# Optimization experiments

Hardware: AMD Instinct MI355X
Metric: run time of the kernel (lower is better)

The kernel has to match this reference:

```python
import jax, jax.numpy as jnp
import numpy as np

EPS = 1e-5


def setup_inputs() -> dict:
    key = jax.random.key(0)
    k1, k2, k3 = jax.random.split(key, 3)
    B, C, H, W = 64, 512, 28, 28
    G = 8
    x = jax.random.normal(k1, (B, C, H, W), dtype=jnp.float32)
    weight = jax.random.normal(k2, (G,), dtype=jnp.float32)
    bias = jax.random.normal(k3, (G,), dtype=jnp.float32)
    return {"x": x, "weight": weight, "bias": bias, "groups": G}


def reference(x, weight, bias, groups):
    B, C, H, W = x.shape
    G = groups
    cpg = C // G
    hw = H * W
    xg = x.reshape(B, G, cpg, hw)                       # [B,G,cpg,HW]
    # per-channel spatial mean
    means = jnp.mean(xg, axis=-1, keepdims=True)        # [B,G,cpg,1]
    # similarity map: dot product of each spatial vector with channel-mean vector
    s = jnp.sum(xg * means, axis=2)                     # [B,G,HW]
    # normalize s over spatial dim (population variance, eps=1e-5)
    mu = jnp.mean(s, axis=-1, keepdims=True)
    var = jnp.mean(jnp.square(s - mu), axis=-1, keepdims=True)
    t = (s - mu) * jax.lax.rsqrt(var + EPS)             # [B,G,HW]
    gate = jax.nn.sigmoid(t * weight[None, :, None] + bias[None, :, None])
    out = xg * gate[:, :, None, :]                      # broadcast gate over channels
    return out.reshape(B, C, H, W)
```

## Files before the change

kernel.cpp:

```cpp
#include <hip/hip_runtime.h>


#define HW    784
#define HW4   196
#define CPG   64
#define NG    8

__global__ __launch_bounds__(512, 4)
void sge_kernel(const float* __restrict__ x,
                const float* __restrict__ weight,
                const float* __restrict__ bias,
                float* __restrict__ out) {
    __shared__ float means[CPG];
    __shared__ float gate[HW];
    __shared__ float red[16];

    const int t    = threadIdx.x;
    const int lane = t & 63;
    const int wave = t >> 6;
    const int c    = t >> 3;
    const int jj   = t & 7;

    const int bg = blockIdx.x;
    const int g  = bg & (NG - 1);
    const size_t tile4 = (size_t)bg * (CPG * HW4);
    const float4* xp = (const float4*)x + tile4 + (size_t)c * HW4;

    float cs = 0.f;
#pragma unroll
    for (int k = 0; k < 24; ++k) {
        const float4 v = xp[jj + 8 * k];
        cs += (v.x + v.y) + (v.z + v.w);
    }
    if (jj < 4) {
        const float4 v = xp[192 + jj];
        cs += (v.x + v.y) + (v.z + v.w);
    }
    cs += __shfl_xor(cs, 1, 64);
    cs += __shfl_xor(cs, 2, 64);
    cs += __shfl_xor(cs, 4, 64);
    if (jj == 0) means[c] = cs * (1.0f / (float)HW);
    __syncthreads();

    const float* xs = x + (size_t)bg * (CPG * HW);
    const bool  has1 = (t + 512) < HW;
    const int   p1   = has1 ? (t + 512) : t;
    float s0 = 0.f, s1 = 0.f;
#pragma unroll 8
    for (int cc = 0; cc < CPG; ++cc) {
        const float  mc   = means[cc];
        const float* rowp = xs + (size_t)cc * HW;
        s0 += rowp[t]  * mc;
        s1 += rowp[p1] * mc;
    }

    float rs  = s0 + (has1 ? s1 : 0.f);
    float rs2 = s0 * s0 + (has1 ? s1 * s1 : 0.f);
#pragma unroll
    for (int m = 1; m < 64; m <<= 1) {
        rs  += __shfl_xor(rs,  m, 64);
        rs2 += __shfl_xor(rs2, m, 64);
    }
    if (lane == 0) { red[wave] = rs; red[8 + wave] = rs2; }
    __syncthreads();

    float sum_s = 0.f, sum_s2 = 0.f;
#pragma unroll
    for (int w = 0; w < 8; ++w) { sum_s += red[w]; sum_s2 += red[8 + w]; }
    const float mu   = sum_s * (1.0f / (float)HW);
    const float var  = sum_s2 * (1.0f / (float)HW) - mu * mu;
    const float rstd = rsqrtf(var + 1e-5f);
    const float wg   = weight[g];
    const float bgv  = bias[g];

    {
        const float z0 = (s0 - mu) * rstd * wg + bgv;
        gate[t] = 1.0f / (1.0f + __expf(-z0));
        if (has1) {
            const float z1 = (s1 - mu) * rstd * wg + bgv;
            gate[t + 512] = 1.0f / (1.0f + __expf(-z1));
        }
    }
    __syncthreads();

    const float4* g4 = (const float4*)gate;
    float4* op = (float4*)out + tile4 + (size_t)c * HW4;
#pragma unroll
    for (int k = 0; k < 24; ++k) {
        const float4 v  = xp[jj + 8 * k];
        const float4 gv = g4[jj + 8 * k];
        float4 o;
        o.x = v.x * gv.x; o.y = v.y * gv.y;
        o.z = v.z * gv.z; o.w = v.w * gv.w;
        op[jj + 8 * k] = o;
    }
    if (jj < 4) {
        const float4 v  = xp[192 + jj];
        const float4 gv = g4[192 + jj];
        float4 o;
        o.x = v.x * gv.x; o.y = v.y * gv.y;
        o.z = v.z * gv.z; o.w = v.w * gv.w;
        op[192 + jj] = o;
    }
}

extern "C" void kernel_launch(void* const* d_in, const int* in_sizes, int n_in,
                              void* d_out, int out_size, void* d_ws, size_t ws_size,
                              hipStream_t stream) {
    const float* x      = (const float*)d_in[0];
    const float* weight = (const float*)d_in[1];
    const float* bias   = (const float*)d_in[2];
    float* out = (float*)d_out;
    sge_kernel<<<dim3(512), dim3(512), 0, stream>>>(x, weight, bias, out);
}
```

Baseline: 207.0 us.

## Split fused SGE kernel into means, gate, and grid-stride multiply kernels

Replaces the single per-(batch,group) fused kernel, which ran only 512 blocks, with three kernels. One wave computes each channel mean, a per-group kernel computes and stores the gate map in workspace, and a grid-stride elementwise kernel applies the gate using nontemporal stores. The aim is more parallelism and occupancy in the mean and multiply phases. In exchange it adds two kernel launches, a workspace round trip for means and gates, and extra full reads of x that may no longer hit cache.

Result: slower. 227.8 us (+10.0%).

```diff
diff --git a/kernel.cpp b/kernel.cpp
--- a/kernel.cpp
+++ b/kernel.cpp
@@ -5,102 +5,113 @@
 #define HW4   196
 #define CPG   64
 #define NG    8
+#define NROWS (64 * 512)
+#define TOT4  (NROWS * HW4)
 
-__global__ __launch_bounds__(512, 4)
-void sge_kernel(const float* __restrict__ x,
-                const float* __restrict__ weight,
-                const float* __restrict__ bias,
-                float* __restrict__ out) {
-    __shared__ float means[CPG];
-    __shared__ float gate[HW];
-    __shared__ float red[16];
+typedef float f32x4 __attribute__((ext_vector_type(4)));
+
+__global__ __launch_bounds__(256)
+void k_means(const float* __restrict__ x, float* __restrict__ means) {
+    const int t    = threadIdx.x;
+    const int lane = t & 63;
+    const int row  = blockIdx.x * 4 + (t >> 6);
+    const float4* xp = (const float4*)x + (size_t)row * HW4;
+
+    const float4 v0 = xp[lane];
+    const float4 v1 = xp[lane + 64];
+    const float4 v2 = xp[lane + 128];
+    float s = ((v0.x + v0.y) + (v0.z + v0.w))
+            + ((v1.x + v1.y) + (v1.z + v1.w))
+            + ((v2.x + v2.y) + (v2.z + v2.w));
+    if (lane < 4) {
+        const float4 v3 = xp[192 + lane];
+        s += (v3.x + v3.y) + (v3.z + v3.w);
+    }
+#pragma unroll
+    for (int m = 1; m < 64; m <<= 1) s += __shfl_xor(s, m, 64);
+    if (lane == 0) means[row] = s * (1.0f / (float)HW);
+}
+
+__global__ __launch_bounds__(256)
+void k_gate(const float* __restrict__ x, const float* __restrict__ means,
+            const float* __restrict__ weight, const float* __restrict__ bias,
+            float* __restrict__ gate) {
+    __shared__ float mloc[CPG];
+    __shared__ float red[8];
 
     const int t    = threadIdx.x;
     const int lane = t & 63;
     const int wave = t >> 6;
-    const int c    = t >> 3;
-    const int jj   = t & 7;
+    const int bg   = blockIdx.x;
+    const int g    = bg & (NG - 1);
 
-    const int bg = blockIdx.x;
-    const int g  = bg & (NG - 1);
-    const size_t tile4 = (size_t)bg * (CPG * HW4);
-    const float4* xp = (const float4*)x + tile4 + (size_t)c * HW4;
-
-    float cs = 0.f;
-#pragma unroll
-    for (int k = 0; k < 24; ++k) {
-        const float4 v = xp[jj + 8 * k];
-        cs += (v.x + v.y) + (v.z + v.w);
-    }
-    if (jj < 4) {
-        const float4 v = xp[192 + jj];
-        cs += (v.x + v.y) + (v.z + v.w);
-    }
-    cs += __shfl_xor(cs, 1, 64);
-    cs += __shfl_xor(cs, 2, 64);
-    cs += __shfl_xor(cs, 4, 64);
-    if (jj == 0) means[c] = cs * (1.0f / (float)HW);
+    if (t < CPG) mloc[t] = means[bg * CPG + t];
     __syncthreads();
 
     const float* xs = x + (size_t)bg * (CPG * HW);
-    const bool  has1 = (t + 512) < HW;
-    const int   p1   = has1 ? (t + 512) : t;
-    float s0 = 0.f, s1 = 0.f;
+    float s0 = 0.f, s1 = 0.f, s2 = 0.f, s3 = 0.f;
 #pragma unroll 8
-    for (int cc = 0; cc < CPG; ++cc) {
-        const float  mc   = means[cc];
-        const float* rowp = xs + (size_t)cc * HW;
-        s0 += rowp[t]  * mc;
-        s1 += rowp[p1] * mc;
+    for (int c = 0; c < CPG; ++c) {
+        const float  mc = mloc[c];
+        const float* rp = xs + c * HW;
+        s0 += rp[t]       * mc;
+        s1 += rp[t + 256] * mc;
+        s2 += rp[t + 512] * mc;
+        if (t < 16) s3 += rp[t + 768] * mc;
     }
 
-    float rs  = s0 + (has1 ? s1 : 0.f);
-    float rs2 = s0 * s0 + (has1 ? s1 * s1 : 0.f);
+    float rs  = s0 + s1 + s2 + s3;
+    float rs2 = s0 * s0 + s1 * s1 + s2 * s2 + s3 * s3;
 #pragma unroll
     for (int m = 1; m < 64; m <<= 1) {
         rs  += __shfl_xor(rs,  m, 64);
         rs2 += __shfl_xor(rs2, m, 64);
     }
-    if (lane == 0) { red[wave] = rs; red[8 + wave] = rs2; }
+    if (lane == 0) { red[wave] = rs; red[4 + wave] = rs2; }
     __syncthreads();
 
-    float sum_s = 0.f, sum_s2 = 0.f;
-#pragma unroll
-    for (int w = 0; w < 8; ++w) { sum_s += red[w]; sum_s2 += red[8 + w]; }
+    const float sum_s  = red[0] + red[1] + red[2] + red[3];
+    const float sum_s2 = red[4] + red[5] + red[6] + red[7];
     const float mu   = sum_s * (1.0f / (float)HW);
     const float var  = sum_s2 * (1.0f / (float)HW) - mu * mu;
     const float rstd = rsqrtf(var + 1e-5f);
     const float wg   = weight[g];
     const float bgv  = bias[g];
 
+    float* gr = gate + (size_t)bg * HW;
     {
         const float z0 = (s0 - mu) * rstd * wg + bgv;
-        gate[t] = 1.0f / (1.0f + __expf(-z0));
-        if (has1) {
-            const float z1 = (s1 - mu) * rstd * wg + bgv;
-            gate[t + 512] = 1.0f / (1.0f + __expf(-z1));
+        const float z1 = (s1 - mu) * rstd * wg + bgv;
+        const float z2 = (s2 - mu) * rstd * wg + bgv;
+        gr[t]       = 1.0f / (1.0f + __expf(-z0));
+        gr[t + 256] = 1.0f / (1.0f + __expf(-z1));
+        gr[t + 512] = 1.0f / (1.0f + __expf(-z2));
+        if (t < 16) {
+            const float z3 = (s3 - mu) * rstd * wg + bgv;
+            gr[t + 768] = 1.0f / (1.0f + __expf(-z3));
         }
     }
-    __syncthreads();
+}
 
+__global__ __launch_bounds__(256)
+void k_mul(const float* __restrict__ x, const float* __restrict__ gate,
+           float* __restrict__ out) {
+    const int tid    = blockIdx.x * 256 + threadIdx.x;
+    const int stride = gridDim.x * 256;
+    const float4* x4 = (const float4*)x;
     const float4* g4 = (const float4*)gate;
-    float4* op = (float4*)out + tile4 + (size_t)c * HW4;
-#pragma unroll
-    for (int k = 0; k < 24; ++k) {
-        const float4 v  = xp[jj + 8 * k];
-        const float4 gv = g4[jj + 8 * k];
-        float4 o;
+    f32x4*        o4 = (f32x4*)out;
+
+    for (int i = tid; i < TOT4; i += stride) {
+        const int row = i / HW4;
+        const int h4  = i - row * HW4;
+        const int bg  = row >> 6;
+        const float4 v  = x4[i];
+        const float4 gv = g4[bg * HW4 + h4];
+        f32x4 o;
         o.x = v.x * gv.x; o.y = v.y * gv.y;
         o.z = v.z * gv.z; o.w = v.w * gv.w;
-        op[jj + 8 * k] = o;
-    }
-    if (jj < 4) {
-        const float4 v  = xp[192 + jj];
-        const float4 gv = g4[192 + jj];
-        float4 o;
-        o.x = v.x * gv.x; o.y = v.y * gv.y;
-        o.z = v.z * gv.z; o.w = v.w * gv.w;
-        op[192 + jj] = o;
+        __builtin_nontemporal_store(o, &o4[i]);
     }
 }
 
@@ -110,6 +121,11 @@
     const float* x      = (const float*)d_in[0];
     const float* weight = (const float*)d_in[1];
     const float* bias   = (const float*)d_in[2];
-    float* out = (float*)d_out;
-    sge_kernel<<<dim3(512), dim3(512), 0, stream>>>(x, weight, bias, out);
+    float* out   = (float*)d_out;
+    float* gate  = (float*)d_ws;
+    float* means = (float*)((char*)d_ws + 1605632);
+
+    k_means<<<dim3(NROWS / 4), dim3(256), 0, stream>>>(x, means);
+    k_gate <<<dim3(512),       dim3(256), 0, stream>>>(x, means, weight, bias, gate);
+    k_mul  <<<dim3(4096),      dim3(256), 0, stream>>>(x, gate, out);
 }
```

## Stage 8-channel slabs in LDS with register double-buffering for fused mean/similarity pass

Applied to the files above, without the earlier changes.

Restructures the first two passes so the tile is streamed once in chunks of 8 channels. Each chunk is loaded into registers, copied into a double-buffered LDS stage, and then used for both the per-channel mean and the accumulation of the similarity dot product. Before, x was read from global memory twice ahead of the gating pass. The output pass now uses flat coalesced indexing with non-temporal stores. The trade-offs are about 50KB of LDS per block, which cuts occupancy below the launch-bounds target, and two barriers per chunk.

Measured after the change: 213.1 us. 1.03x slower.

```diff
diff --git a/kernel.cpp b/kernel.cpp
--- a/kernel.cpp
+++ b/kernel.cpp
@@ -1,61 +1,101 @@
 #include <hip/hip_runtime.h>
 
 
-#define HW    784
-#define HW4   196
-#define CPG   64
-#define NG    8
+#define HW     784
+#define HW4    196
+#define NG     8
+#define TILE4  12544
+#define EF4    1568
+#define NE     8
+
+typedef float f32x4 __attribute__((ext_vector_type(4)));
 
 __global__ __launch_bounds__(512, 4)
 void sge_kernel(const float* __restrict__ x,
                 const float* __restrict__ weight,
                 const float* __restrict__ bias,
                 float* __restrict__ out) {
-    __shared__ float means[CPG];
-    __shared__ float gate[HW];
+    __shared__ float stage[2][8 * HW];
+    __shared__ float gbuf[HW];
+    __shared__ float smean[8];
     __shared__ float red[16];
 
     const int t    = threadIdx.x;
     const int lane = t & 63;
     const int wave = t >> 6;
-    const int c    = t >> 3;
-    const int jj   = t & 7;
+    const int bg   = blockIdx.x;
+    const int g    = bg & (NG - 1);
 
-    const int bg = blockIdx.x;
-    const int g  = bg & (NG - 1);
-    const size_t tile4 = (size_t)bg * (CPG * HW4);
-    const float4* xp = (const float4*)x + tile4 + (size_t)c * HW4;
+    const float4* xt = (const float4*)x + (size_t)bg * TILE4;
 
-    float cs = 0.f;
+    const bool x3   = (t < (EF4 - 3 * 512));
+    const bool has1 = (t < (HW - 512));
+
+    float4 a0, a1, a2, a3, b0, b1, b2, b3;
+    float acc0 = 0.f, acc1 = 0.f;
+
+    a0 = xt[t]; a1 = xt[t + 512]; a2 = xt[t + 1024];
+    if (x3) a3 = xt[t + 1536];
+
+    for (int e = 0; e < NE; ++e) {
+        float4* sh = (float4*)stage[e & 1];
+        if ((e & 1) == 0) {
+            sh[t] = a0; sh[t + 512] = a1; sh[t + 1024] = a2;
+            if (x3) sh[t + 1536] = a3;
+            if (e + 1 < NE) {
+                const float4* src = xt + (e + 1) * EF4;
+                b0 = src[t]; b1 = src[t + 512]; b2 = src[t + 1024];
+                if (x3) b3 = src[t + 1536];
+            }
+        } else {
+            sh[t] = b0; sh[t + 512] = b1; sh[t + 1024] = b2;
+            if (x3) sh[t + 1536] = b3;
+            if (e + 1 < NE) {
+                const float4* src = xt + (e + 1) * EF4;
+                a0 = src[t]; a1 = src[t + 512]; a2 = src[t + 1024];
+                if (x3) a3 = src[t + 1536];
+            }
+        }
+        __syncthreads();
+
+        {
+            const float4* row4 = (const float4*)(stage[e & 1] + wave * HW);
+            const float4 v0 = row4[lane];
+            const float4 v1 = row4[lane + 64];
+            const float4 v2 = row4[lane + 128];
+            float s = ((v0.x + v0.y) + (v0.z + v0.w))
+                    + ((v1.x + v1.y) + (v1.z + v1.w))
+                    + ((v2.x + v2.y) + (v2.z + v2.w));
+            if (lane < 4) {
+                const float4 v3 = row4[lane + 192];
+                s += (v3.x + v3.y) + (v3.z + v3.w);
+            }
 #pragma unroll
-    for (int k = 0; k < 24; ++k) {
-        const float4 v = xp[jj + 8 * k];
-        cs += (v.x + v.y) + (v.z + v.w);
-    }
-    if (jj < 4) {
-        const float4 v = xp[192 + jj];
-        cs += (v.x + v.y) + (v.z + v.w);
-    }
-    cs += __shfl_xor(cs, 1, 64);
-    cs += __shfl_xor(cs, 2, 64);
-    cs += __shfl_xor(cs, 4, 64);
-    if (jj == 0) means[c] = cs * (1.0f / (float)HW);
-    __syncthreads();
+            for (int m = 1; m < 64; m <<= 1) s += __shfl_xor(s, m, 64);
+            if (lane == 0) smean[wave] = s * (1.0f / (float)HW);
+        }
+        __syncthreads();
 
-    const float* xs = x + (size_t)bg * (CPG * HW);
-    const bool  has1 = (t + 512) < HW;
-    const int   p1   = has1 ? (t + 512) : t;
-    float s0 = 0.f, s1 = 0.f;
-#pragma unroll 8
-    for (int cc = 0; cc < CPG; ++cc) {
-        const float  mc   = means[cc];
-        const float* rowp = xs + (size_t)cc * HW;
-        s0 += rowp[t]  * mc;
-        s1 += rowp[p1] * mc;
+        {
+            const float* sb = stage[e & 1];
+            const float m0 = smean[0], m1 = smean[1], m2 = smean[2], m3 = smean[3];
+            const float m4 = smean[4], m5 = smean[5], m6 = smean[6], m7 = smean[7];
+            acc0 += sb[t]          * m0 + sb[t + HW]     * m1
+                  + sb[t + 2 * HW] * m2 + sb[t + 3 * HW] * m3
+                  + sb[t + 4 * HW] * m4 + sb[t + 5 * HW] * m5
+                  + sb[t + 6 * HW] * m6 + sb[t + 7 * HW] * m7;
+            if (has1) {
+                const int p = t + 512;
+                acc1 += sb[p]          * m0 + sb[p + HW]     * m1
+                      + sb[p + 2 * HW] * m2 + sb[p + 3 * HW] * m3
+                      + sb[p + 4 * HW] * m4 + sb[p + 5 * HW] * m5
+                      + sb[p + 6 * HW] * m6 + sb[p + 7 * HW] * m7;
+            }
+        }
     }
 
-    float rs  = s0 + (has1 ? s1 : 0.f);
-    float rs2 = s0 * s0 + (has1 ? s1 * s1 : 0.f);
+    float rs  = acc0 + (has1 ? acc1 : 0.f);
+    float rs2 = acc0 * acc0 + (has1 ? acc1 * acc1 : 0.f);
 #pragma unroll
     for (int m = 1; m < 64; m <<= 1) {
         rs  += __shfl_xor(rs,  m, 64);
@@ -71,36 +111,37 @@
     const float var  = sum_s2 * (1.0f / (float)HW) - mu * mu;
     const float rstd = rsqrtf(var + 1e-5f);
     const float wg   = weight[g];
-    const float bgv  = bias[g];
+    const float bv   = bias[g];
 
     {
-        const float z0 = (s0 - mu) * rstd * wg + bgv;
-        gate[t] = 1.0f / (1.0f + __expf(-z0));
+        const float z0 = (acc0 - mu) * rstd * wg + bv;
+        gbuf[t] = 1.0f / (1.0f + __expf(-z0));
         if (has1) {
-            const float z1 = (s1 - mu) * rstd * wg + bgv;
-            gate[t + 512] = 1.0f / (1.0f + __expf(-z1));
+            const float z1 = (acc1 - mu) * rstd * wg + bv;
+            gbuf[t + 512] = 1.0f / (1.0f + __expf(-z1));
         }
     }
     __syncthreads();
 
-    const float4* g4 = (const float4*)gate;
-    float4* op = (float4*)out + tile4 + (size_t)c * HW4;
+    const f32x4* x4  = (const f32x4*)x + (size_t)bg * TILE4;
+    f32x4*       o4  = (f32x4*)out + (size_t)bg * TILE4;
+    const f32x4* gb4 = (const f32x4*)gbuf;
+
+    int q = t % HW4;
 #pragma unroll
-    for (int k = 0; k < 24; ++k) {
-        const float4 v  = xp[jj + 8 * k];
-        const float4 gv = g4[jj + 8 * k];
-        float4 o;
-        o.x = v.x * gv.x; o.y = v.y * gv.y;
-        o.z = v.z * gv.z; o.w = v.w * gv.w;
-        op[jj + 8 * k] = o;
+    for (int r = 0; r < 24; ++r) {
+        const int idx = t + r * 512;
+        const f32x4 v  = x4[idx];
+        const f32x4 gv = gb4[q];
+        const f32x4 o  = v * gv;
+        __builtin_nontemporal_store(o, &o4[idx]);
+        q += 120; if (q >= HW4) q -= HW4;
     }
-    if (jj < 4) {
-        const float4 v  = xp[192 + jj];
-        const float4 gv = g4[192 + jj];
-        float4 o;
-        o.x = v.x * gv.x; o.y = v.y * gv.y;
-        o.z = v.z * gv.z; o.w = v.w * gv.w;
-        op[192 + jj] = o;
+    if (t < 256) {
+        const int idx = 12288 + t;
+        const f32x4 v = x4[idx];
+        const f32x4 o = v * gb4[idx % HW4];
+        __builtin_nontemporal_store(o, &o4[idx]);
     }
 }
 
```
